# Kernel tuning notes

Measured on AMD Instinct MI355X. Metric: run time of the kernel, lower is better.

Reference implementation:

```python
import jax, jax.numpy as jnp
import numpy as np

# Model dims (see ModelArgs: d_model=1024, expand=2, d_state=16, dt_rank=ceil(1024/16), d_conv=4)
D_MODEL = 1024
D_INNER = 2048
D_STATE = 16
DT_RANK = 64
D_CONV = 4
N_LAYER = 2
VOCAB = 50280  # 50277 padded to multiple of 8
B, L = 1, 1024
EPS = 1e-5


def setup_inputs() -> dict:
    key = jax.random.key(0)
    ks = jax.random.split(key, 12)
    nrm = lambda k, shape, s: (jax.random.normal(k, shape) * s).astype(jnp.float32)
    A = jnp.tile(jnp.arange(1, D_STATE + 1, dtype=jnp.float32), (N_LAYER, D_INNER, 1))
    return {
        "input_ids": jax.random.randint(ks[0], (B, L), 0, VOCAB, dtype=jnp.int32),
        "embedding": nrm(ks[1], (VOCAB, D_MODEL), 0.02),
        "norm_scale": jnp.ones((N_LAYER, D_MODEL), jnp.float32) + nrm(ks[2], (N_LAYER, D_MODEL), 0.02),
        "in_proj_w": nrm(ks[3], (N_LAYER, D_MODEL, 2 * D_INNER), D_MODEL ** -0.5),
        "conv_w": nrm(ks[4], (N_LAYER, D_CONV, D_INNER), D_CONV ** -0.5),
        "conv_b": nrm(ks[5], (N_LAYER, D_INNER), 0.02),
        "x_proj_w": nrm(ks[6], (N_LAYER, D_INNER, DT_RANK + 2 * D_STATE), D_INNER ** -0.5),
        "dt_proj_w": nrm(ks[7], (N_LAYER, DT_RANK, D_INNER), DT_RANK ** -0.5),
        "dt_proj_b": nrm(ks[8], (N_LAYER, D_INNER), 0.02),
        "A_log": jnp.log(A),
        "D_skip": jnp.ones((N_LAYER, D_INNER), jnp.float32),
        "out_proj_w": nrm(ks[9], (N_LAYER, D_INNER, D_MODEL), D_INNER ** -0.5),
        "norm_f_scale": jnp.ones((D_MODEL,), jnp.float32),
    }


def _rmsnorm(x, scale):
    return x * jax.lax.rsqrt(jnp.mean(jnp.square(x), axis=-1, keepdims=True) + EPS) * scale


def _selective_scan(u, delta, A, Bm, Cm, Dp):
    # u, delta: [b,l,d]; A: [d,n]; Bm, Cm: [b,l,n]; Dp: [d]
    deltaA = jnp.exp(jnp.einsum('bld,dn->bldn', delta, A))          # [b,l,d,n]
    dBu = jnp.einsum('bld,bln,bld->bldn', delta, Bm, u)             # [b,l,d,n]

    def step(h, xs):
        dA_t, dBu_t, C_t = xs                                       # [b,d,n],[b,d,n],[b,n]
        h = dA_t * h + dBu_t
        return h, jnp.einsum('bdn,bn->bd', h, C_t)

    h0 = jnp.zeros((u.shape[0], u.shape[2], A.shape[1]), u.dtype)
    _, ys = jax.lax.scan(step, h0, (jnp.swapaxes(deltaA, 0, 1),
                                    jnp.swapaxes(dBu, 0, 1),
                                    jnp.swapaxes(Cm, 0, 1)))
    y = jnp.swapaxes(ys, 0, 1)                                      # [b,l,d]
    return y + u * Dp


def _mamba_block(x, in_w, cw, cb, xp_w, dt_w, dt_b, A_log, Dp, out_w):
    xr = x @ in_w                                                   # [b,l,2*d_inner], no bias
    xc, res = xr[..., :D_INNER], xr[..., D_INNER:]
    # depthwise causal conv: flax pads (K-1) both sides then takes [:, :l] == left-pad K-1
    k = cw[:, None, :]                                              # [K, 1, d_inner] (WIO)
    xc = jax.lax.conv_general_dilated(
        xc, k, window_strides=(1,), padding=[(D_CONV - 1, 0)],
        dimension_numbers=('NWC', 'WIO', 'NWC'), feature_group_count=D_INNER) + cb
    xc = jax.nn.silu(xc)
    A = -jnp.exp(A_log)
    x_dbl = xc @ xp_w                                               # [b,l,dt_rank+2n]
    dt = x_dbl[..., :DT_RANK]
    Bm = x_dbl[..., DT_RANK:DT_RANK + D_STATE]
    Cm = x_dbl[..., DT_RANK + D_STATE:]
    delta = jax.nn.softplus(dt @ dt_w + dt_b)                       # [b,l,d_inner]
    y = _selective_scan(xc, delta, A, Bm, Cm, Dp)
    y = y * jax.nn.silu(res)
    return y @ out_w


def reference(input_ids, embedding, norm_scale, in_proj_w, conv_w, conv_b,
              x_proj_w, dt_proj_w, dt_proj_b, A_log, D_skip, out_proj_w, norm_f_scale):
    x = embedding[input_ids]                                        # [b,l,d_model]

    def layer(x, lp):
        ns, in_w, cw, cb, xpw, dtw, dtb, al, dp, ow = lp
        return x + _mamba_block(_rmsnorm(x, ns), in_w, cw, cb, xpw, dtw, dtb, al, dp, ow), None

    x, _ = jax.lax.scan(layer, x, (norm_scale, in_proj_w, conv_w, conv_b, x_proj_w,
                                   dt_proj_w, dt_proj_b, A_log, D_skip, out_proj_w))
    x = _rmsnorm(x, norm_f_scale)
    return x @ embedding.T                                          # tied lm_head (embedding.attend)
```

## Files before the change

kernel.cpp:

```cpp
#include <hip/hip_runtime.h>

#define DM    1024
#define DI    2048
#define DS    16
#define DTR   64
#define DCONV 4
#define NLAY  2
#define NVOCAB 50280
#define SEQ   1024
#define REPS  1e-5f

typedef unsigned short u16;
typedef short bf16x8 __attribute__((ext_vector_type(8)));
typedef float f32x4 __attribute__((ext_vector_type(4)));

__device__ __forceinline__ u16 bf16_rn(float f) {
  unsigned int u = __float_as_uint(f);
  return (u16)((u + 0x7fffu + ((u >> 16) & 1u)) >> 16);
}
__device__ __forceinline__ float bf16_to_f(u16 h) {
  return __uint_as_float((unsigned int)h << 16);
}
__device__ __forceinline__ float silu_f(float x) { return x / (1.f + __expf(-x)); }

__global__ void k_embed(const int* __restrict__ ids, const float* __restrict__ E,
                        float* __restrict__ x) {
  int t = blockIdx.x;
  int c = threadIdx.x * 4;
  float4 v = *(const float4*)&E[(size_t)ids[t] * DM + c];
  *(float4*)&x[(size_t)t * DM + c] = v;
}

__global__ void k_rmsnorm(const float* __restrict__ x, const float* __restrict__ sc,
                          u16* __restrict__ hi, u16* __restrict__ lo) {
  int t = blockIdx.x, tid = threadIdx.x;
  float4 v = *(const float4*)&x[(size_t)t * DM + tid * 4];
  float s = v.x * v.x + v.y * v.y + v.z * v.z + v.w * v.w;
  for (int o = 32; o; o >>= 1) s += __shfl_xor(s, o);
  __shared__ float red[4];
  if ((tid & 63) == 0) red[tid >> 6] = s;
  __syncthreads();
  float tot = red[0] + red[1] + red[2] + red[3];
  float r = rsqrtf(tot / (float)DM + REPS);
  int c = tid * 4;
  float f[4] = {v.x * r * sc[c + 0], v.y * r * sc[c + 1],
                v.z * r * sc[c + 2], v.w * r * sc[c + 3]};
  unsigned long long ph = 0, pl = 0;
#pragma unroll
  for (int i = 0; i < 4; i++) {
    u16 h = bf16_rn(f[i]);
    u16 l = bf16_rn(f[i] - bf16_to_f(h));
    ph |= (unsigned long long)h << (16 * i);
    pl |= (unsigned long long)l << (16 * i);
  }
  *(unsigned long long*)&hi[(size_t)t * DM + c] = ph;
  *(unsigned long long*)&lo[(size_t)t * DM + c] = pl;
}

struct TDesc { const float* src; u16* dhi; u16* dlo; int R, C, tstart; };
struct TPack { TDesc d[4]; };

__global__ void k_transpose(TPack p) {
  __shared__ float tile[32][33];
  int bt = blockIdx.x;
  int di = 0;
#pragma unroll
  for (int i = 1; i < 4; i++) if (bt >= p.d[i].tstart) di = i;
  TDesc d = p.d[di];
  int tloc = bt - d.tstart;
  int tpc = d.C >> 5;
  int r0 = (tloc / tpc) * 32, c0 = (tloc % tpc) * 32;
  int tx = threadIdx.x & 31, ty = threadIdx.x >> 5;
#pragma unroll
  for (int i = 0; i < 4; i++) {
    int r = ty + i * 8;
    tile[r][tx] = d.src[(size_t)(r0 + r) * d.C + c0 + tx];
  }
  __syncthreads();
#pragma unroll
  for (int i = 0; i < 4; i++) {
    int cr = ty + i * 8;
    float v = tile[tx][cr];
    u16 h = bf16_rn(v);
    size_t off = (size_t)(c0 + cr) * d.R + r0 + tx;
    d.dhi[off] = h;
    d.dlo[off] = bf16_rn(v - bf16_to_f(h));
  }
}

__global__ void k_conv(const float* __restrict__ xr, const float* __restrict__ cw,
                       const float* __restrict__ cb, float* __restrict__ xc) {
  int i = blockIdx.x * 256 + threadIdx.x;
  int t = i >> 11, d = i & (DI - 1);
  float acc = cb[d];
#pragma unroll
  for (int k = 0; k < DCONV; k++) {
    int tt = t - (DCONV - 1) + k;
    if (tt >= 0) acc = fmaf(cw[k * DI + d], xr[(size_t)tt * (2 * DI) + d], acc);
  }
  xc[i] = silu_f(acc);
}

__global__ void k_xdbl(const float* __restrict__ xc, const float* __restrict__ W,
                       float* __restrict__ xdbl) {
  __shared__ float rows[4][DI];
  int t0 = blockIdx.x * 4, tid = threadIdx.x;
#pragma unroll
  for (int it = 0; it < 16; it++) {
    int idx = it * 128 + tid;
    int r = idx >> 9, c = (idx & 511) * 4;
    *(float4*)&rows[r][c] = *(const float4*)&xc[(size_t)(t0 + r) * DI + c];
  }
  __syncthreads();
  int j = tid;
  if (j >= 96) return;
  float acc0 = 0.f, acc1 = 0.f, acc2 = 0.f, acc3 = 0.f;
#pragma unroll 4
  for (int k = 0; k < DI; k++) {
    float w = W[(size_t)k * 96 + j];
    acc0 = fmaf(rows[0][k], w, acc0);
    acc1 = fmaf(rows[1][k], w, acc1);
    acc2 = fmaf(rows[2][k], w, acc2);
    acc3 = fmaf(rows[3][k], w, acc3);
  }
  xdbl[(size_t)(t0 + 0) * 128 + j] = acc0;
  xdbl[(size_t)(t0 + 1) * 128 + j] = acc1;
  xdbl[(size_t)(t0 + 2) * 128 + j] = acc2;
  xdbl[(size_t)(t0 + 3) * 128 + j] = acc3;
}

__global__ void k_dtproj(const float* __restrict__ xdbl, const float* __restrict__ W,
                         const float* __restrict__ b, float* __restrict__ delta) {
  __shared__ float dt[4][DTR];
  int t0 = blockIdx.x * 4;
  int d = blockIdx.y * 256 + threadIdx.x;
  int tid = threadIdx.x;
  {
    int r = tid >> 6, k = tid & 63;
    dt[r][k] = xdbl[(size_t)(t0 + r) * 128 + k];
  }
  __syncthreads();
  float bias = b[d];
  float acc0 = bias, acc1 = bias, acc2 = bias, acc3 = bias;
#pragma unroll
  for (int k = 0; k < DTR; k++) {
    float w = W[(size_t)k * DI + d];
    acc0 = fmaf(dt[0][k], w, acc0);
    acc1 = fmaf(dt[1][k], w, acc1);
    acc2 = fmaf(dt[2][k], w, acc2);
    acc3 = fmaf(dt[3][k], w, acc3);
  }
  float a[4] = {acc0, acc1, acc2, acc3};
#pragma unroll
  for (int r = 0; r < 4; r++) {
    float v = a[r];
    delta[(size_t)(t0 + r) * DI + d] = (v > 20.f) ? v : log1pf(__expf(v));
  }
}

__global__ void k_scan(const float* __restrict__ delta, const float* __restrict__ xdbl,
                       const float* __restrict__ u, const float* __restrict__ A_log,
                       const float* __restrict__ Dskip, float* __restrict__ y) {
  int n = threadIdx.x & 15, dl = threadIdx.x >> 4;
  int d = blockIdx.x * 16 + dl;
  float An = -__expf(A_log[d * DS + n]);
  float Dd = Dskip[d];
  float h = 0.f;
  float del = delta[d], uu = u[d];
  float Bn = xdbl[64 + n], Cn = xdbl[80 + n];
  for (int t = 0; t < SEQ; t++) {
    float del2 = 0.f, uu2 = 0.f, Bn2 = 0.f, Cn2 = 0.f;
    if (t + 1 < SEQ) {
      del2 = delta[(size_t)(t + 1) * DI + d];
      uu2 = u[(size_t)(t + 1) * DI + d];
      Bn2 = xdbl[(t + 1) * 128 + 64 + n];
      Cn2 = xdbl[(t + 1) * 128 + 80 + n];
    }
    float dA = __expf(del * An);
    h = fmaf(dA, h, del * Bn * uu);
    float p = h * Cn;
    p += __shfl_xor(p, 8);
    p += __shfl_xor(p, 4);
    p += __shfl_xor(p, 2);
    p += __shfl_xor(p, 1);
    if (n == 0) y[(size_t)t * DI + d] = fmaf(uu, Dd, p);
    del = del2; uu = uu2; Bn = Bn2; Cn = Cn2;
  }
}

__global__ void k_y2(const float* __restrict__ y, const float* __restrict__ xr,
                     u16* __restrict__ hi, u16* __restrict__ lo) {
  int i = blockIdx.x * 256 + threadIdx.x;
  int t = i >> 11, d = i & (DI - 1);
  float r = xr[(size_t)t * (2 * DI) + DI + d];
  float v = y[i] * silu_f(r);
  u16 h = bf16_rn(v);
  hi[i] = h;
  lo[i] = bf16_rn(v - bf16_to_f(h));
}

#define EPI_STORE 0
#define EPI_ADD 1

__device__ __forceinline__ void async16(const u16* g, u16* l) {
  __builtin_amdgcn_global_load_lds(
      (const __attribute__((address_space(1))) unsigned int*)g,
      (__attribute__((address_space(3))) unsigned int*)l, 16, 0, 0);
}

template <int EPI, bool BF32, bool NGUARD>
__launch_bounds__(256)
__global__ void k_gemm(const u16* __restrict__ A, const void* __restrict__ Bt,
                       float* __restrict__ C, int M, int N, int K,
                       int ldA, int ldB, int ldC, int Mb) {
  __shared__ u16 lds_a[128 * 32];
  __shared__ u16 lds_b[128 * 32];
  int bx = blockIdx.x;
  int m0 = (bx % Mb) * 128;
  int n0 = (bx / Mb) * 128;
  int tid = threadIdx.x, ln = tid & 63;
  int wv = tid >> 6, wm = wv >> 1, wn = wv & 1;
  int ml = ln & 15, q = ln >> 4;

  f32x4 zero = {0.f, 0.f, 0.f, 0.f};
  f32x4 acc[4][4];
#pragma unroll
  for (int i = 0; i < 4; i++)
#pragma unroll
    for (int j = 0; j < 4; j++) acc[i][j] = zero;

  for (int k0 = 0; k0 < K; k0 += 32) {
    __syncthreads();
#pragma unroll
    for (int r = 0; r < 2; r++) {
      int idx = r * 256 + tid;
      const u16* g = A + (size_t)(m0 + (idx >> 2)) * ldA + k0 + (idx & 3) * 8;
      u16* l = lds_a + (size_t)(r * 256 + (tid & ~63)) * 8;
      async16(g, l);
    }
    if (!BF32) {
#pragma unroll
      for (int r = 0; r < 2; r++) {
        int idx = r * 256 + tid;
        const u16* g = (const u16*)Bt + (size_t)(n0 + (idx >> 2)) * ldB + k0 + (idx & 3) * 8;
        u16* l = lds_b + (size_t)(r * 256 + (tid & ~63)) * 8;
        async16(g, l);
      }
    } else {
#pragma unroll
      for (int r = 0; r < 4; r++) {
        int idx = r * 256 + tid;
        int row = idx >> 3, cg = idx & 7;
        int nr = n0 + row;
        if (NGUARD) nr = min(nr, N - 1);
        float4 v = *(const float4*)((const float*)Bt + (size_t)nr * ldB + k0 + cg * 4);
        unsigned long long pk =
            (unsigned long long)bf16_rn(v.x) |
            ((unsigned long long)bf16_rn(v.y) << 16) |
            ((unsigned long long)bf16_rn(v.z) << 32) |
            ((unsigned long long)bf16_rn(v.w) << 48);
        *(unsigned long long*)&lds_b[row * 32 + cg * 4] = pk;
      }
    }
    __syncthreads();

    bf16x8 af[4], bfr[4];
#pragma unroll
    for (int i = 0; i < 4; i++)
      af[i] = *(const bf16x8*)&lds_a[(wm * 64 + i * 16 + ml) * 32 + q * 8];
#pragma unroll
    for (int j = 0; j < 4; j++)
      bfr[j] = *(const bf16x8*)&lds_b[(wn * 64 + j * 16 + ml) * 32 + q * 8];
#pragma unroll
    for (int i = 0; i < 4; i++)
#pragma unroll
      for (int j = 0; j < 4; j++)
        acc[i][j] = __builtin_amdgcn_mfma_f32_16x16x32_bf16(af[i], bfr[j], acc[i][j], 0, 0, 0);
  }

#pragma unroll
  for (int i = 0; i < 4; i++)
#pragma unroll
    for (int j = 0; j < 4; j++) {
      int c = n0 + wn * 64 + j * 16 + ml;
      if (NGUARD && c >= N) continue;
      int rbase = m0 + wm * 64 + i * 16 + q * 4;
#pragma unroll
      for (int rg = 0; rg < 4; rg++) {
        int r = rbase + rg;
        float v = acc[i][j][rg];
        size_t off = (size_t)r * ldC + c;
        if (EPI == EPI_STORE) C[off] = v;
        else C[off] += v;
      }
    }
}

extern "C" void kernel_launch(void* const* d_in, const int* in_sizes, int n_in,
                              void* d_out, int out_size, void* d_ws, size_t ws_size,
                              hipStream_t stream) {
  const int* ids = (const int*)d_in[0];
  const float* E = (const float*)d_in[1];
  const float* norm_scale = (const float*)d_in[2];
  const float* in_proj_w = (const float*)d_in[3];
  const float* conv_w = (const float*)d_in[4];
  const float* conv_b = (const float*)d_in[5];
  const float* x_proj_w = (const float*)d_in[6];
  const float* dt_proj_w = (const float*)d_in[7];
  const float* dt_proj_b = (const float*)d_in[8];
  const float* A_log = (const float*)d_in[9];
  const float* D_skip = (const float*)d_in[10];
  const float* out_proj_w = (const float*)d_in[11];
  const float* norm_f_scale = (const float*)d_in[12];
  float* out = (float*)d_out;

  char* p = (char*)d_ws;
  auto alloc = [&](size_t bytes) { char* r = p; p += (bytes + 255) & ~(size_t)255; return r; };
  float* x = (float*)alloc((size_t)SEQ * DM * 4);
  u16* xn_h = (u16*)alloc((size_t)SEQ * DM * 2);
  u16* xn_l = (u16*)alloc((size_t)SEQ * DM * 2);
  float* xr = (float*)alloc((size_t)SEQ * 2 * DI * 4);
  float* xc = (float*)alloc((size_t)SEQ * DI * 4);
  float* xdbl = (float*)alloc((size_t)SEQ * 128 * 4);
  float* delta = (float*)alloc((size_t)SEQ * DI * 4);
  float* ybuf = (float*)alloc((size_t)SEQ * DI * 4);
  u16* y2h = (u16*)alloc((size_t)SEQ * DI * 2);
  u16* y2l = (u16*)alloc((size_t)SEQ * DI * 2);
  u16* xf_h = (u16*)alloc((size_t)SEQ * DM * 2);
  u16* xf_l = (u16*)alloc((size_t)SEQ * DM * 2);
  u16 *inTh[NLAY], *inTl[NLAY], *outTh[NLAY], *outTl[NLAY];
  for (int l = 0; l < NLAY; l++) {
    inTh[l] = (u16*)alloc((size_t)(2 * DI) * DM * 2);
    inTl[l] = (u16*)alloc((size_t)(2 * DI) * DM * 2);
    outTh[l] = (u16*)alloc((size_t)DM * DI * 2);
    outTl[l] = (u16*)alloc((size_t)DM * DI * 2);
  }

  TPack pk;
  int ts = 0;
  for (int l = 0; l < NLAY; l++) {
    pk.d[l * 2 + 0] = {in_proj_w + (size_t)l * DM * 2 * DI, inTh[l], inTl[l], DM, 2 * DI, ts};
    ts += (DM / 32) * (2 * DI / 32);
    pk.d[l * 2 + 1] = {out_proj_w + (size_t)l * DI * DM, outTh[l], outTl[l], DI, DM, ts};
    ts += (DI / 32) * (DM / 32);
  }
  k_transpose<<<ts, 256, 0, stream>>>(pk);

  k_embed<<<SEQ, 256, 0, stream>>>(ids, E, x);

  for (int l = 0; l < NLAY; l++) {
    k_rmsnorm<<<SEQ, 256, 0, stream>>>(x, norm_scale + (size_t)l * DM, xn_h, xn_l);
    k_gemm<EPI_STORE, false, false><<<8 * 32, 256, 0, stream>>>(
        xn_h, inTh[l], xr, SEQ, 2 * DI, DM, DM, DM, 2 * DI, 8);
    k_gemm<EPI_ADD, false, false><<<8 * 32, 256, 0, stream>>>(
        xn_l, inTh[l], xr, SEQ, 2 * DI, DM, DM, DM, 2 * DI, 8);
    k_gemm<EPI_ADD, false, false><<<8 * 32, 256, 0, stream>>>(
        xn_h, inTl[l], xr, SEQ, 2 * DI, DM, DM, DM, 2 * DI, 8);
    k_conv<<<(SEQ * DI) / 256, 256, 0, stream>>>(
        xr, conv_w + (size_t)l * DCONV * DI, conv_b + (size_t)l * DI, xc);
    k_xdbl<<<SEQ / 4, 128, 0, stream>>>(xc, x_proj_w + (size_t)l * DI * 96, xdbl);
    {
      dim3 g(SEQ / 4, DI / 256);
      k_dtproj<<<g, 256, 0, stream>>>(xdbl, dt_proj_w + (size_t)l * DTR * DI,
                                      dt_proj_b + (size_t)l * DI, delta);
    }
    k_scan<<<DI / 16, 256, 0, stream>>>(delta, xdbl, xc,
                                        A_log + (size_t)l * DI * DS,
                                        D_skip + (size_t)l * DI, ybuf);
    k_y2<<<(SEQ * DI) / 256, 256, 0, stream>>>(ybuf, xr, y2h, y2l);
    k_gemm<EPI_ADD, false, false><<<8 * 8, 256, 0, stream>>>(
        y2h, outTh[l], x, SEQ, DM, DI, DI, DI, DM, 8);
    k_gemm<EPI_ADD, false, false><<<8 * 8, 256, 0, stream>>>(
        y2l, outTh[l], x, SEQ, DM, DI, DI, DI, DM, 8);
    k_gemm<EPI_ADD, false, false><<<8 * 8, 256, 0, stream>>>(
        y2h, outTl[l], x, SEQ, DM, DI, DI, DI, DM, 8);
  }

  k_rmsnorm<<<SEQ, 256, 0, stream>>>(x, norm_f_scale, xf_h, xf_l);
  int nblk = (NVOCAB + 127) / 128;
  k_gemm<EPI_STORE, true, true><<<8 * nblk, 256, 0, stream>>>(
      xf_h, E, out, SEQ, NVOCAB, DM, DM, DM, NVOCAB, 8);
}
```

Baseline: 2.357 ms.

## Fuse split-bf16 three-pass GEMMs into one kernel and add XCD block swizzle

Replaces the three separate hi/lo bf16 GEMM launches (hi*hi, lo*hi, hi*lo) for the in_proj and out_proj with a single kernel that loads all four operand tiles and issues three MFMAs per tile. This removes two launches and two extra read-modify-write passes over the fp32 output per projection, and reuses the loaded A/B tiles. A block-index swizzle is also added so that consecutive tiles are grouped per XCD, intended to improve L2 locality, and it applies to the lm_head GEMM as well. The trade-off is doubled LDS use and more registers per block, which may lower occupancy. The swizzle assumes the grid size is a multiple of 8, otherwise it leaves some tiles uncomputed; the lm_head grid of 8*393 satisfies this.

```diff
diff --git a/kernel.cpp b/kernel.cpp
--- a/kernel.cpp
+++ b/kernel.cpp
@@ -208,6 +208,10 @@
       (__attribute__((address_space(3))) unsigned int*)l, 16, 0, 0);
 }
 
+__device__ __forceinline__ int xcd_swz(int bx, int nwg) {
+  return (bx & 7) * (nwg >> 3) + (bx >> 3);
+}
+
 template <int EPI, bool BF32, bool NGUARD>
 __launch_bounds__(256)
 __global__ void k_gemm(const u16* __restrict__ A, const void* __restrict__ Bt,
@@ -215,7 +219,7 @@
                        int ldA, int ldB, int ldC, int Mb) {
   __shared__ u16 lds_a[128 * 32];
   __shared__ u16 lds_b[128 * 32];
-  int bx = blockIdx.x;
+  int bx = xcd_swz(blockIdx.x, gridDim.x);
   int m0 = (bx % Mb) * 128;
   int n0 = (bx / Mb) * 128;
   int tid = threadIdx.x, ln = tid & 63;
@@ -284,6 +288,85 @@
     for (int j = 0; j < 4; j++) {
       int c = n0 + wn * 64 + j * 16 + ml;
       if (NGUARD && c >= N) continue;
+      int rbase = m0 + wm * 64 + i * 16 + q * 4;
+#pragma unroll
+      for (int rg = 0; rg < 4; rg++) {
+        int r = rbase + rg;
+        float v = acc[i][j][rg];
+        size_t off = (size_t)r * ldC + c;
+        if (EPI == EPI_STORE) C[off] = v;
+        else C[off] += v;
+      }
+    }
+}
+
+template <int EPI>
+__launch_bounds__(256)
+__global__ void k_gemm3(const u16* __restrict__ Ah, const u16* __restrict__ Al,
+                        const u16* __restrict__ Bh, const u16* __restrict__ Bl,
+                        float* __restrict__ C, int M, int N, int K,
+                        int ldA, int ldB, int ldC, int Mb) {
+  __shared__ u16 lds_ah[128 * 32];
+  __shared__ u16 lds_al[128 * 32];
+  __shared__ u16 lds_bh[128 * 32];
+  __shared__ u16 lds_bl[128 * 32];
+  int bx = xcd_swz(blockIdx.x, gridDim.x);
+  int m0 = (bx % Mb) * 128;
+  int n0 = (bx / Mb) * 128;
+  int tid = threadIdx.x, ln = tid & 63;
+  int wv = tid >> 6, wm = wv >> 1, wn = wv & 1;
+  int ml = ln & 15, q = ln >> 4;
+
+  f32x4 zero = {0.f, 0.f, 0.f, 0.f};
+  f32x4 acc[4][4];
+#pragma unroll
+  for (int i = 0; i < 4; i++)
+#pragma unroll
+    for (int j = 0; j < 4; j++) acc[i][j] = zero;
+
+  for (int k0 = 0; k0 < K; k0 += 32) {
+    __syncthreads();
+#pragma unroll
+    for (int r = 0; r < 2; r++) {
+      int idx = r * 256 + tid;
+      size_t goffA = (size_t)(m0 + (idx >> 2)) * ldA + k0 + (idx & 3) * 8;
+      size_t goffB = (size_t)(n0 + (idx >> 2)) * ldB + k0 + (idx & 3) * 8;
+      size_t loff = (size_t)(r * 256 + (tid & ~63)) * 8;
+      async16(Ah + goffA, lds_ah + loff);
+      async16(Al + goffA, lds_al + loff);
+      async16(Bh + goffB, lds_bh + loff);
+      async16(Bl + goffB, lds_bl + loff);
+    }
+    __syncthreads();
+
+    bf16x8 ah[4], al[4], bh[4], bl[4];
+#pragma unroll
+    for (int i = 0; i < 4; i++) {
+      int ro = (wm * 64 + i * 16 + ml) * 32 + q * 8;
+      ah[i] = *(const bf16x8*)&lds_ah[ro];
+      al[i] = *(const bf16x8*)&lds_al[ro];
+    }
+#pragma unroll
+    for (int j = 0; j < 4; j++) {
+      int ro = (wn * 64 + j * 16 + ml) * 32 + q * 8;
+      bh[j] = *(const bf16x8*)&lds_bh[ro];
+      bl[j] = *(const bf16x8*)&lds_bl[ro];
+    }
+#pragma unroll
+    for (int i = 0; i < 4; i++)
+#pragma unroll
+      for (int j = 0; j < 4; j++) {
+        acc[i][j] = __builtin_amdgcn_mfma_f32_16x16x32_bf16(ah[i], bh[j], acc[i][j], 0, 0, 0);
+        acc[i][j] = __builtin_amdgcn_mfma_f32_16x16x32_bf16(al[i], bh[j], acc[i][j], 0, 0, 0);
+        acc[i][j] = __builtin_amdgcn_mfma_f32_16x16x32_bf16(ah[i], bl[j], acc[i][j], 0, 0, 0);
+      }
+  }
+
+#pragma unroll
+  for (int i = 0; i < 4; i++)
+#pragma unroll
+    for (int j = 0; j < 4; j++) {
+      int c = n0 + wn * 64 + j * 16 + ml;
       int rbase = m0 + wm * 64 + i * 16 + q * 4;
 #pragma unroll
       for (int rg = 0; rg < 4; rg++) {
@@ -350,12 +433,8 @@
 
   for (int l = 0; l < NLAY; l++) {
     k_rmsnorm<<<SEQ, 256, 0, stream>>>(x, norm_scale + (size_t)l * DM, xn_h, xn_l);
-    k_gemm<EPI_STORE, false, false><<<8 * 32, 256, 0, stream>>>(
-        xn_h, inTh[l], xr, SEQ, 2 * DI, DM, DM, DM, 2 * DI, 8);
-    k_gemm<EPI_ADD, false, false><<<8 * 32, 256, 0, stream>>>(
-        xn_l, inTh[l], xr, SEQ, 2 * DI, DM, DM, DM, 2 * DI, 8);
-    k_gemm<EPI_ADD, false, false><<<8 * 32, 256, 0, stream>>>(
-        xn_h, inTl[l], xr, SEQ, 2 * DI, DM, DM, DM, 2 * DI, 8);
+    k_gemm3<EPI_STORE><<<8 * 32, 256, 0, stream>>>(
+        xn_h, xn_l, inTh[l], inTl[l], xr, SEQ, 2 * DI, DM, DM, DM, 2 * DI, 8);
     k_conv<<<(SEQ * DI) / 256, 256, 0, stream>>>(
         xr, conv_w + (size_t)l * DCONV * DI, conv_b + (size_t)l * DI, xc);
     k_xdbl<<<SEQ / 4, 128, 0, stream>>>(xc, x_proj_w + (size_t)l * DI * 96, xdbl);
@@ -368,12 +447,8 @@
                                         A_log + (size_t)l * DI * DS,
                                         D_skip + (size_t)l * DI, ybuf);
     k_y2<<<(SEQ * DI) / 256, 256, 0, stream>>>(ybuf, xr, y2h, y2l);
-    k_gemm<EPI_ADD, false, false><<<8 * 8, 256, 0, stream>>>(
-        y2h, outTh[l], x, SEQ, DM, DI, DI, DI, DM, 8);
-    k_gemm<EPI_ADD, false, false><<<8 * 8, 256, 0, stream>>>(
-        y2l, outTh[l], x, SEQ, DM, DI, DI, DI, DM, 8);
-    k_gemm<EPI_ADD, false, false><<<8 * 8, 256, 0, stream>>>(
-        y2h, outTl[l], x, SEQ, DM, DI, DI, DI, DM, 8);
+    k_gemm3<EPI_ADD><<<8 * 8, 256, 0, stream>>>(
+        y2h, y2l, outTh[l], outTl[l], x, SEQ, DM, DI, DI, DI, DM, 8);
   }
 
   k_rmsnorm<<<SEQ, 256, 0, stream>>>(x, norm_f_scale, xf_h, xf_l);
```

Result: faster. 2.066 ms (-12.3%).
